# Kernel tuning notes

Measured on AMD Instinct MI355X. Metric: run time of the kernel, lower is better.

The kernel has to match this reference:

```python
import jax, jax.numpy as jnp
import numpy as np

B, N, T = 1, 1024, 2048   # batch, graph nodes, timesteps
E, K = 16384, 32          # edges, causal kernel taps


def setup_inputs() -> dict:
    key = jax.random.key(0)
    k1, k2, k3, k4 = jax.random.split(key, 4)
    x = jax.random.normal(k1, (B, N, T), dtype=jnp.float32)
    # per-edge causal impulse-response kernels (aggregator(g) output)
    kernel = jax.random.normal(k2, (E, K), dtype=jnp.float32) * 0.1
    src = jax.random.randint(k3, (E,), 0, N)
    dst = jax.random.randint(k4, (E,), 0, N)
    return {"x": x, "kernel": kernel, "src": src, "dst": dst}


def reference(x, kernel, src, dst):
    # Block-sparse causal conv over the edge list:
    #   y_e[b, t] = sum_k kernel[e, k] * x[b, src_e, t - k]   (causal)
    #   out[b, n, t] = x[b, n, t] + sum_{e: dst_e = n} y_e[b, t]
    # (residual applied because g.include_index_diag is False)
    xs = x[:, src, :]                      # [B, E, T] gather upstream signals
    rhs = kernel[:, None, ::-1]            # [E, 1, K] flipped -> true causal conv
    y = jax.lax.conv_general_dilated(
        xs, rhs,
        window_strides=(1,),
        padding=[(K - 1, 0)],              # left-pad: strictly causal
        dimension_numbers=("NCW", "OIW", "NCW"),
        feature_group_count=E,             # one independent kernel per edge
    )                                      # [B, E, T]
    agg = jax.ops.segment_sum(jnp.swapaxes(y, 0, 1), dst, num_segments=N)  # [N, B, T]
    return x + jnp.swapaxes(agg, 0, 1)     # [B, N, T]
```

## Files before the change

kernel.cpp:

```cpp
#include <hip/hip_runtime.h>
#include <hip/hip_bf16.h>

#define TT  2048
#define KK  32
#define NN  1024
#define EE  16384
#define CAP 64

typedef short short8  __attribute__((ext_vector_type(8)));
typedef short short4v __attribute__((ext_vector_type(4)));
typedef float f32x4   __attribute__((ext_vector_type(4)));

__device__ short g_xbf[NN * TT];
__device__ short g_kbf[EE * KK];

__device__ __forceinline__ short f2bf(float f) {
    __hip_bfloat16 h = __float2bfloat16(f);
    return __builtin_bit_cast(short, h);
}

__device__ __forceinline__ void gload_lds16(const short* g, short* l) {
    __builtin_amdgcn_global_load_lds(
        (const __attribute__((address_space(1))) void*)(const void*)(g),
        (__attribute__((address_space(3))) void*)(void*)(l), 16, 0, 0);
}

__global__ __launch_bounds__(256) void prep_kernel(const float* __restrict__ x,
                                                   const float* __restrict__ kern) {
    const int bid = blockIdx.x;
    if (bid < NN) {
        const int i = bid * 256 + threadIdx.x;
        const float4* x4 = (const float4*)x;
        const float4 a = x4[2 * i], b = x4[2 * i + 1];
        short8 h;
        h[0]=f2bf(a.x); h[1]=f2bf(a.y); h[2]=f2bf(a.z); h[3]=f2bf(a.w);
        h[4]=f2bf(b.x); h[5]=f2bf(b.y); h[6]=f2bf(b.z); h[7]=f2bf(b.w);
        ((short8*)g_xbf)[i] = h;
    } else {
        const int i = (bid - NN) * 256 + threadIdx.x;
        const float4* k4 = (const float4*)kern;
        const float4 a = k4[2 * i], b = k4[2 * i + 1];
        short8 h;
        h[0]=f2bf(a.x); h[1]=f2bf(a.y); h[2]=f2bf(a.z); h[3]=f2bf(a.w);
        h[4]=f2bf(b.x); h[5]=f2bf(b.y); h[6]=f2bf(b.z); h[7]=f2bf(b.w);
        ((short8*)g_kbf)[i] = h;
    }
}

__global__ __launch_bounds__(512, 8) void lti_kernel(
    const float* __restrict__ x,
    const int*   __restrict__ src,
    const int*   __restrict__ dst,
    float*       __restrict__ out)
{
    const int n   = blockIdx.x;
    const int tid = threadIdx.x;
    const int v   = tid >> 6;
    const int w   = v & 3;
    const int q   = v >> 2;
    const int ln  = tid & 63;
    const int c   = ln & 15, g = ln >> 4;
    const int t0  = 512 * w;

    __shared__ __align__(16) short xs_all[8][3][544];
    __shared__ __align__(16) short kt_all[8][8][72];
    __shared__ __align__(16) short dummy[32];
    __shared__ int bl[CAP];
    __shared__ int bc;

    short (*xsb)[544] = xs_all[v];
    short (*kt)[72]   = kt_all[v];

    short8 z8; z8[0]=0;z8[1]=0;z8[2]=0;z8[3]=0;z8[4]=0;z8[5]=0;z8[6]=0;z8[7]=0;

    if (tid == 0) bc = 0;
    {
        short8* kz = (short8*)&kt[0][0];
        kz[ln] = z8;
        if (ln < 8) kz[64 + ln] = z8;
        if (w == 0 && ln < 12) *(short8*)&xsb[ln >> 2][8 * (ln & 3)] = z8;
    }
    __syncthreads();

    const int4* d4 = (const int4*)dst;
    #pragma unroll
    for (int it = 0; it < EE / 2048; ++it) {
        const int i4 = tid + 512 * it;
        const int4 d = d4[i4];
        const int eb = 4 * i4;
        if (d.x == n) { int p = atomicAdd(&bc, 1); if (p < CAP) bl[p] = (src[eb    ] << 14) | (eb    ); }
        if (d.y == n) { int p = atomicAdd(&bc, 1); if (p < CAP) bl[p] = (src[eb + 1] << 14) | (eb + 1); }
        if (d.z == n) { int p = atomicAdd(&bc, 1); if (p < CAP) bl[p] = (src[eb + 2] << 14) | (eb + 2); }
        if (d.w == n) { int p = atomicAdd(&bc, 1); if (p < CAP) bl[p] = (src[eb + 3] << 14) | (eb + 3); }
    }
    __syncthreads();
    int L = bc; if (L > CAP) L = CAP;
    const int M = (L - q + 1) >> 1;
    #define IDX(I) (q + 2 * (I))

    f32x4 acc0 = {0,0,0,0}, acc1 = {0,0,0,0};
    short4v tr0, tr1, tr2;

    short* hdst = w ? (short*)nullptr : dummy;

    const int a_ = c & 7;
    const int s1 = ((a_ + 1) & 7) + 15 - c + 8 * g;

    #define ISSUE(S, P)                                                                \
    {                                                                                  \
        const unsigned sv = (unsigned)bl[P];                                           \
        const int e0 = __builtin_amdgcn_readfirstlane((int)(sv & 16383u));             \
        const int s0 = __builtin_amdgcn_readfirstlane((int)(sv >> 14));                \
        const short* rb = g_xbf + (size_t)s0 * TT;                                     \
        gload_lds16(rb + t0 + 8 * ln, &xsb[S][32]);                                    \
        if (ln < 4)                                                                    \
            gload_lds16(rb + (w ? t0 - 32 : 0) + 8 * ln, w ? &xsb[S][0] : dummy);      \
        tr##S = *(const short4v*)(g_kbf + ((size_t)e0 << 5) + 4 * (ln & 7));           \
    }

    #define COMMIT(S)                                                                  \
    {                                                                                  \
        const int a2 = ln >> 3, pad = (a2 + 1) & 7, mb = 4 * (ln & 7);                 \
        kt[a2][pad + 47 - mb] = tr##S[0];                                              \
        kt[a2][pad + 46 - mb] = tr##S[1];                                              \
        kt[a2][pad + 45 - mb] = tr##S[2];                                              \
        kt[a2][pad + 44 - mb] = tr##S[3];                                              \
    }

    #define COMPUTE(S)                                                                 \
    {                                                                                  \
        const short8 b1 = *(const short8*)&kt[a_][s1];                                 \
        short8 b2 = *(const short8*)&kt[a_][s1 + 16];                                  \
        if (g < 2) b2 = z8;                              \
        {                                                                              \
            const short8 a1  = *(const short8*)&xsb[S][16 * c + 8 * g];                \
            const short8 a2v = *(const short8*)&xsb[S][16 * c + 8 * g + 16];           \
            acc0 = __builtin_amdgcn_mfma_f32_16x16x32_bf16(a1,  b1, acc0, 0, 0, 0);    \
            acc0 = __builtin_amdgcn_mfma_f32_16x16x32_bf16(a2v, b2, acc0, 0, 0, 0);    \
        }                                                                              \
        {                                                                              \
            const short8 a1  = *(const short8*)&xsb[S][256 + 16 * c + 8 * g];          \
            const short8 a2v = *(const short8*)&xsb[S][256 + 16 * c + 8 * g + 16];     \
            acc1 = __builtin_amdgcn_mfma_f32_16x16x32_bf16(a1,  b1, acc1, 0, 0, 0);    \
            acc1 = __builtin_amdgcn_mfma_f32_16x16x32_bf16(a2v, b2, acc1, 0, 0, 0);    \
        }                                                                              \
    }

    #define BODY(SC, SN, I)                                                            \
    if ((I) < M) {                                                                     \
        __builtin_amdgcn_sched_barrier(0);                                             \
        if ((I) + 2 < M) ISSUE(SN, IDX((I) + 2));                                      \
        const int rem = M - (I);                                                       \
        if (rem >= 3)      { asm volatile("s_waitcnt vmcnt(6)" ::: "memory"); }        \
        else if (rem == 2) { asm volatile("s_waitcnt vmcnt(3)" ::: "memory"); }        \
        else               { asm volatile("s_waitcnt vmcnt(0)" ::: "memory"); }        \
        __builtin_amdgcn_sched_barrier(0);                                             \
        COMMIT(SC);                                                                    \
        COMPUTE(SC);                                                                   \
    }

    if (M > 0) ISSUE(0, IDX(0));
    if (M > 1) ISSUE(1, IDX(1));
    for (int i = 0; i < M; i += 3) {
        BODY(0, 2, i);
        BODY(1, 0, i + 1);
        BODY(2, 1, i + 2);
    }

    if (q == 1) {
        float* rd = (float*)&xs_all[v][0][0];
        #pragma unroll
        for (int qd = 0; qd < 4; ++qd) {
            const int ta = 64 * g + 16 * qd + c;
            rd[ta]       = acc0[qd];
            rd[256 + ta] = acc1[qd];
        }
    }
    __syncthreads();
    if (q == 0) {
        const float* rd  = (const float*)&xs_all[v + 4][0][0];
        const float* xr  = x   + (size_t)n * TT + t0;
        float*       orw = out + (size_t)n * TT + t0;
        #pragma unroll
        for (int qd = 0; qd < 4; ++qd) {
            const int ta = 64 * g + 16 * qd + c;
            orw[ta]       = xr[ta]       + acc0[qd] + rd[ta];
            orw[256 + ta] = xr[256 + ta] + acc1[qd] + rd[256 + ta];
        }
    }
    #undef IDX
    #undef ISSUE
    #undef COMMIT
    #undef COMPUTE
    #undef BODY
}

extern "C" void kernel_launch(void* const* d_in, const int* in_sizes, int n_in,
                              void* d_out, int out_size, void* d_ws, size_t ws_size,
                              hipStream_t stream) {
    const float* x    = (const float*)d_in[0];
    const float* kern = (const float*)d_in[1];
    const int*   src  = (const int*)d_in[2];
    const int*   dst  = (const int*)d_in[3];
    float*       out  = (float*)d_out;

    prep_kernel<<<dim3(NN + EE * KK / 8 / 256), dim3(256), 0, stream>>>(x, kern);
    lti_kernel<<<dim3(NN), dim3(512), 0, stream>>>(x, src, dst, out);
}
```

Measured before the change: 42.23 us.

## Build per-node edge buckets in a separate pass and split blocks per time tile

Each block previously scanned the full 16K-entry dst array to find its incoming edges. A global atomic bucketing kernel now builds per-node slot lists once, and the main kernel just loads them. The main grid also changes from 1024 blocks of 512 threads to 4096 blocks of 256, one block per node and time tile. Inside each block, four waves split the edges and reduce through shared memory with a vectorized epilogue. This adds a kernel launch, a counter-zeroing step, and global atomics, and slot order within a bucket becomes nondeterministic.

```diff
diff --git a/kernel.cpp b/kernel.cpp
--- a/kernel.cpp
+++ b/kernel.cpp
@@ -25,8 +25,9 @@
         (__attribute__((address_space(3))) void*)(void*)(l), 16, 0, 0);
 }
 
-__global__ __launch_bounds__(256) void prep_kernel(const float* __restrict__ x,
-                                                   const float* __restrict__ kern) {
+__global__ __launch_bounds__(256) void cvt_kernel(const float* __restrict__ x,
+                                                  const float* __restrict__ kern,
+                                                  int* __restrict__ cnt) {
     const int bid = blockIdx.x;
     if (bid < NN) {
         const int i = bid * 256 + threadIdx.x;
@@ -36,7 +37,7 @@
         h[0]=f2bf(a.x); h[1]=f2bf(a.y); h[2]=f2bf(a.z); h[3]=f2bf(a.w);
         h[4]=f2bf(b.x); h[5]=f2bf(b.y); h[6]=f2bf(b.z); h[7]=f2bf(b.w);
         ((short8*)g_xbf)[i] = h;
-    } else {
+    } else if (bid < NN + 256) {
         const int i = (bid - NN) * 256 + threadIdx.x;
         const float4* k4 = (const float4*)kern;
         const float4 a = k4[2 * i], b = k4[2 * i + 1];
@@ -44,71 +45,70 @@
         h[0]=f2bf(a.x); h[1]=f2bf(a.y); h[2]=f2bf(a.z); h[3]=f2bf(a.w);
         h[4]=f2bf(b.x); h[5]=f2bf(b.y); h[6]=f2bf(b.z); h[7]=f2bf(b.w);
         ((short8*)g_kbf)[i] = h;
-    }
-}
-
-__global__ __launch_bounds__(512, 8) void lti_kernel(
-    const float* __restrict__ x,
-    const int*   __restrict__ src,
-    const int*   __restrict__ dst,
-    float*       __restrict__ out)
+    } else {
+        int4* c4 = (int4*)cnt;
+        c4[threadIdx.x] = make_int4(0, 0, 0, 0);
+    }
+}
+
+__global__ __launch_bounds__(256) void csr_kernel(const int* __restrict__ src,
+                                                  const int* __restrict__ dst,
+                                                  int* __restrict__ cnt,
+                                                  unsigned* __restrict__ slots) {
+    const int e = blockIdx.x * 256 + threadIdx.x;
+    const int d = dst[e];
+    const int p = atomicAdd(&cnt[d], 1);
+    if (p < CAP) slots[(size_t)d * CAP + p] = ((unsigned)src[e] << 14) | (unsigned)e;
+}
+
+__global__ __launch_bounds__(256, 6) void lti_kernel(
+    const float*    __restrict__ x,
+    const int*      __restrict__ cnt,
+    const unsigned* __restrict__ slots,
+    float*          __restrict__ out)
 {
-    const int n   = blockIdx.x;
+    const int bid = blockIdx.x;
+    const int w   = bid >> 10;
+    const int n   = bid & 1023;
     const int tid = threadIdx.x;
-    const int v   = tid >> 6;
-    const int w   = v & 3;
-    const int q   = v >> 2;
+    const int q   = tid >> 6;
     const int ln  = tid & 63;
     const int c   = ln & 15, g = ln >> 4;
     const int t0  = 512 * w;
 
-    __shared__ __align__(16) short xs_all[8][3][544];
-    __shared__ __align__(16) short kt_all[8][8][72];
+    __shared__ __align__(16) short xs_all[4][3][544];
+    __shared__ __align__(16) short kt_all[4][8][72];
+    __shared__ __align__(16) float red[4][512];
     __shared__ __align__(16) short dummy[32];
-    __shared__ int bl[CAP];
-    __shared__ int bc;
-
-    short (*xsb)[544] = xs_all[v];
-    short (*kt)[72]   = kt_all[v];
+    __shared__ unsigned bl[CAP];
+
+    short (*xsb)[544] = xs_all[q];
+    short (*kt)[72]   = kt_all[q];
 
     short8 z8; z8[0]=0;z8[1]=0;z8[2]=0;z8[3]=0;z8[4]=0;z8[5]=0;z8[6]=0;z8[7]=0;
 
-    if (tid == 0) bc = 0;
     {
         short8* kz = (short8*)&kt[0][0];
         kz[ln] = z8;
         if (ln < 8) kz[64 + ln] = z8;
         if (w == 0 && ln < 12) *(short8*)&xsb[ln >> 2][8 * (ln & 3)] = z8;
     }
+    if (tid < CAP) bl[tid] = slots[(size_t)n * CAP + tid];
+    int L = cnt[n]; if (L > CAP) L = CAP;
     __syncthreads();
 
-    const int4* d4 = (const int4*)dst;
-    #pragma unroll
-    for (int it = 0; it < EE / 2048; ++it) {
-        const int i4 = tid + 512 * it;
-        const int4 d = d4[i4];
-        const int eb = 4 * i4;
-        if (d.x == n) { int p = atomicAdd(&bc, 1); if (p < CAP) bl[p] = (src[eb    ] << 14) | (eb    ); }
-        if (d.y == n) { int p = atomicAdd(&bc, 1); if (p < CAP) bl[p] = (src[eb + 1] << 14) | (eb + 1); }
-        if (d.z == n) { int p = atomicAdd(&bc, 1); if (p < CAP) bl[p] = (src[eb + 2] << 14) | (eb + 2); }
-        if (d.w == n) { int p = atomicAdd(&bc, 1); if (p < CAP) bl[p] = (src[eb + 3] << 14) | (eb + 3); }
-    }
-    __syncthreads();
-    int L = bc; if (L > CAP) L = CAP;
-    const int M = (L - q + 1) >> 1;
-    #define IDX(I) (q + 2 * (I))
+    const int M = (L - q + 3) >> 2;
+    #define IDX(I) (q + 4 * (I))
 
     f32x4 acc0 = {0,0,0,0}, acc1 = {0,0,0,0};
     short4v tr0, tr1, tr2;
 
-    short* hdst = w ? (short*)nullptr : dummy;
-
     const int a_ = c & 7;
     const int s1 = ((a_ + 1) & 7) + 15 - c + 8 * g;
 
     #define ISSUE(S, P)                                                                \
     {                                                                                  \
-        const unsigned sv = (unsigned)bl[P];                                           \
+        const unsigned sv = bl[P];                                                     \
         const int e0 = __builtin_amdgcn_readfirstlane((int)(sv & 16383u));             \
         const int s0 = __builtin_amdgcn_readfirstlane((int)(sv >> 14));                \
         const short* rb = g_xbf + (size_t)s0 * TT;                                     \
@@ -159,16 +159,18 @@
         COMPUTE(SC);                                                                   \
     }
 
-    if (M > 0) ISSUE(0, IDX(0));
-    if (M > 1) ISSUE(1, IDX(1));
-    for (int i = 0; i < M; i += 3) {
-        BODY(0, 2, i);
-        BODY(1, 0, i + 1);
-        BODY(2, 1, i + 2);
-    }
-
-    if (q == 1) {
-        float* rd = (float*)&xs_all[v][0][0];
+    if (M > 0) {
+        ISSUE(0, IDX(0));
+        if (M > 1) ISSUE(1, IDX(1));
+        for (int i = 0; i < M; i += 3) {
+            BODY(0, 2, i);
+            BODY(1, 0, i + 1);
+            BODY(2, 1, i + 2);
+        }
+    }
+
+    {
+        float* rd = &red[q][0];
         #pragma unroll
         for (int qd = 0; qd < 4; ++qd) {
             const int ta = 64 * g + 16 * qd + c;
@@ -177,16 +179,17 @@
         }
     }
     __syncthreads();
-    if (q == 0) {
-        const float* rd  = (const float*)&xs_all[v + 4][0][0];
-        const float* xr  = x   + (size_t)n * TT + t0;
-        float*       orw = out + (size_t)n * TT + t0;
-        #pragma unroll
-        for (int qd = 0; qd < 4; ++qd) {
-            const int ta = 64 * g + 16 * qd + c;
-            orw[ta]       = xr[ta]       + acc0[qd] + rd[ta];
-            orw[256 + ta] = xr[256 + ta] + acc1[qd] + rd[256 + ta];
-        }
+    {
+        const int u = 2 * tid;
+        const float2 r0 = *(const float2*)&red[0][u];
+        const float2 r1 = *(const float2*)&red[1][u];
+        const float2 r2 = *(const float2*)&red[2][u];
+        const float2 r3 = *(const float2*)&red[3][u];
+        const float2 xv = *(const float2*)(x + (size_t)n * TT + t0 + u);
+        float2 o;
+        o.x = xv.x + r0.x + r1.x + r2.x + r3.x;
+        o.y = xv.y + r0.y + r1.y + r2.y + r3.y;
+        *(float2*)(out + (size_t)n * TT + t0 + u) = o;
     }
     #undef IDX
     #undef ISSUE
@@ -204,6 +207,10 @@
     const int*   dst  = (const int*)d_in[3];
     float*       out  = (float*)d_out;
 
-    prep_kernel<<<dim3(NN + EE * KK / 8 / 256), dim3(256), 0, stream>>>(x, kern);
-    lti_kernel<<<dim3(NN), dim3(512), 0, stream>>>(x, src, dst, out);
-}
+    int*      cnt   = (int*)d_ws;
+    unsigned* slots = (unsigned*)((char*)d_ws + 4096);
+
+    cvt_kernel<<<dim3(NN + 256 + 1), dim3(256), 0, stream>>>(x, kern, cnt);
+    csr_kernel<<<dim3(EE / 256), dim3(256), 0, stream>>>(src, dst, cnt, slots);
+    lti_kernel<<<dim3(4 * NN), dim3(256), 0, stream>>>(x, cnt, slots, out);
+}
```

After: 42.16 us. About the same (-0.2%).
